# Performance work log

Measured on AMD Instinct MI355X. Metric: run time of the kernel, lower is better.

The kernel has to match this reference:

```python
import jax, jax.numpy as jnp
import numpy as np

C_ATOM = 128; C_PAIR = 16; H = 4; DH = 32; BQ = 32; BK = 128
N_ATOMS = 11776; NB = N_ATOMS // BQ; N_TOK = 512
C_TOK = 384; C_TP = 128; C_TP_IN = 32; N_LAYERS = 3

def _ln(x):
    mu = jnp.mean(x, axis=-1, keepdims=True)
    xc = x - mu
    var = jnp.mean(xc * xc, axis=-1, keepdims=True)
    return xc * jax.lax.rsqrt(var + 1e-5)

def setup_inputs():
    key = jax.random.key(0)
    ks = jax.random.split(key, 32)
    rn = lambda k, s, sc=0.02: jax.random.normal(k, s, jnp.float32) * sc
    q_idx = jnp.arange(N_ATOMS, dtype=jnp.int32).reshape(NB, BQ)
    centers = jnp.arange(NB, dtype=jnp.int32) * BQ + BQ // 2
    win = centers[:, None] + jnp.arange(-BK // 2, BK // 2, dtype=jnp.int32)[None, :]
    k_mask = (win >= 0) & (win < N_ATOMS)
    k_idx = jnp.clip(win, 0, N_ATOMS - 1)
    return {
        'atom_feats': jax.random.normal(ks[0], (1, N_ATOMS, C_ATOM), jnp.float32),
        'token_pair_feats': jax.random.normal(ks[1], (1, N_TOK, N_TOK, C_TP_IN), jnp.float32),
        'W_cond': rn(ks[2], (C_ATOM, C_ATOM)),
        'W_ph': rn(ks[3], (C_PAIR, C_ATOM)),
        'W_pw': rn(ks[4], (C_PAIR, C_ATOM)),
        'W_mlp1': rn(ks[5], (C_PAIR, C_PAIR)),
        'W_mlp2': rn(ks[6], (C_PAIR, C_PAIR)),
        'pb_ln_w': jnp.ones((C_PAIR,), jnp.float32),
        'pb_ln_b': jnp.zeros((C_PAIR,), jnp.float32),
        'pb_w': rn(ks[7], (H, C_PAIR)),
        'sln_w': rn(ks[8], (N_LAYERS, 2 * C_ATOM, C_ATOM)),
        'qkv_w': rn(ks[9], (N_LAYERS, 3 * C_ATOM, C_ATOM)),
        'q_bias': rn(ks[10], (N_LAYERS, C_ATOM)),
        'out_w': rn(ks[11], (N_LAYERS, C_ATOM, C_ATOM)),
        'out_b': jnp.zeros((N_LAYERS, C_ATOM), jnp.float32),
        'ada_w': rn(ks[12], (N_LAYERS, 2 * C_ATOM, C_ATOM)),
        'ta_w': rn(ks[13], (N_LAYERS, 4 * C_ATOM, C_ATOM)),
        'tb_w': rn(ks[14], (N_LAYERS, C_ATOM, 2 * C_ATOM)),
        'gate_w': rn(ks[15], (N_LAYERS, C_ATOM, C_ATOM)),
        'gate_b': jnp.full((N_LAYERS, C_ATOM), -2.0, jnp.float32),
        'W_tok': rn(ks[16], (C_TOK, C_ATOM)),
        'W_trunk': rn(ks[17], (C_TOK, C_TOK)),
        'W_struct': rn(ks[18], (C_TOK, C_TOK)),
        'W_pairin': rn(ks[19], (C_TP, C_TP_IN)),
        'W_outer': rn(ks[20], (2 * C_TP, C_TOK)),
        'q_idx': q_idx, 'k_idx': k_idx, 'k_mask': k_mask,
        'atom_to_token': jnp.sort(jax.random.randint(ks[21], (N_ATOMS,), 0, N_TOK, dtype=jnp.int32)),
    }

def _forward(atom_feats, token_pair_feats, W_cond, W_ph, W_pw, W_mlp1, W_mlp2,
             pb_ln_w, pb_ln_b, pb_w, sln_w, qkv_w, q_bias, out_w, out_b,
             ada_w, ta_w, tb_w, gate_w, gate_b, W_tok, W_trunk, W_struct,
             W_pairin, W_outer, q_idx, k_idx, k_mask, atom_to_token):
    c = atom_feats @ W_cond.T                       # [1,N,128] atom conditioning
    s_ln = _ln(c)                                   # shared normed conditioning
    # ---- blocked pair representation + pair-to-bias ----
    cq = jax.nn.relu(s_ln[:, q_idx])                # [1,NB,BQ,128]
    ck = jax.nn.relu(s_ln[:, k_idx])                # [1,NB,BK,128]
    p = (cq @ W_ph.T)[:, :, :, None, :] + (ck @ W_pw.T)[:, :, None, :, :]  # [1,NB,BQ,BK,16]
    p = p + jax.nn.relu(jax.nn.relu(p) @ W_mlp1.T) @ W_mlp2.T
    pb = (_ln(p) * pb_ln_w + pb_ln_b) @ pb_w.T      # [1,NB,BQ,BK,H]
    pb = jnp.transpose(pb, (0, 1, 4, 2, 3))         # [1,NB,H,BQ,BK]
    neg = jnp.where(k_mask[None, :, None, None, :], 0.0, -1e9)
    a = c
    scale = 1.0 / np.sqrt(DH).astype(np.float32)
    for l in range(N_LAYERS):
        # blocked local attention with AdaLN-conditioned input
        gb = s_ln @ sln_w[l].T
        x = jax.nn.sigmoid(gb[..., :C_ATOM]) * _ln(a) + gb[..., C_ATOM:]
        qkv = x @ qkv_w[l].T
        q, k, v = jnp.split(qkv, 3, axis=-1)
        q = (q + q_bias[l]).reshape(1, N_ATOMS, H, DH)
        k = k.reshape(1, N_ATOMS, H, DH)
        v = v.reshape(1, N_ATOMS, H, DH)
        qb = q[:, q_idx]; kb = k[:, k_idx]; vb = v[:, k_idx]
        sc = jnp.einsum('bnqhd,bnkhd->bnhqk', qb, kb) * scale + pb + neg
        att = jax.nn.softmax(sc, axis=-1)
        o = jnp.einsum('bnhqk,bnkhd->bnqhd', att, vb).reshape(1, N_ATOMS, C_ATOM)
        a = a + o @ out_w[l].T + out_b[l]
        # AdaLN-modulated SwiGLU transition with adaLN-zero gate (bias init -2)
        gb2 = s_ln @ ada_w[l].T
        xt = jax.nn.sigmoid(gb2[..., :C_ATOM]) * _ln(a) + gb2[..., C_ATOM:]
        ab = xt @ ta_w[l].T
        g = jax.nn.silu(ab[..., :2 * C_ATOM]) * ab[..., 2 * C_ATOM:]
        h = g @ tb_w[l].T
        gate = jax.nn.sigmoid(s_ln @ gate_w[l].T + gate_b[l])
        a = a + gate * h
    # ---- atom -> token aggregation and output projections ----
    atom_out = jax.nn.relu(a @ W_tok.T)             # [1,N,384]
    sums = jax.ops.segment_sum(atom_out[0], atom_to_token, num_segments=N_TOK)
    cnt = jax.ops.segment_sum(jnp.ones((N_ATOMS,), atom_out.dtype), atom_to_token, num_segments=N_TOK)
    tok = (sums / jnp.maximum(cnt, 1.0)[:, None])[None]  # [1,T,384]
    s_trunk = tok @ W_trunk.T
    s_struct = tok @ W_struct.T
    u = tok @ W_outer.T                              # [1,T,256]
    pair = token_pair_feats @ W_pairin.T + u[..., :C_TP][:, :, None, :] + u[..., C_TP:][:, None, :, :]
    return s_trunk, s_struct, pair

def reference(atom_feats, token_pair_feats, W_cond, W_ph, W_pw, W_mlp1, W_mlp2,
              pb_ln_w, pb_ln_b, pb_w, sln_w, qkv_w, q_bias, out_w, out_b,
              ada_w, ta_w, tb_w, gate_w, gate_b, W_tok, W_trunk, W_struct,
              W_pairin, W_outer, q_idx, k_idx, k_mask, atom_to_token):
    return _forward(atom_feats, token_pair_feats, W_cond, W_ph, W_pw, W_mlp1, W_mlp2,
                    pb_ln_w, pb_ln_b, pb_w, sln_w, qkv_w, q_bias, out_w, out_b,
                    ada_w, ta_w, tb_w, gate_w, gate_b, W_tok, W_trunk, W_struct,
                    W_pairin, W_outer, q_idx, k_idx, k_mask, atom_to_token)
```

## Files before the change

kernel.cpp:

```cpp
#include <hip/hip_runtime.h>
#include <cstddef>

typedef unsigned short u16;
typedef __attribute__((ext_vector_type(8))) short bf8;
typedef __attribute__((ext_vector_type(4))) float f4;
typedef __attribute__((ext_vector_type(4))) unsigned short us4;

#define NATOMS 11776
#define NBLK   368

__device__ __forceinline__ u16 f2b(float x){
  union { float f; unsigned u; } v; v.f = x;
  unsigned r = v.u + 0x7fffu + ((v.u >> 16) & 1u);
  return (u16)(r >> 16);
}
__device__ __forceinline__ float b2f(u16 x){
  union { unsigned u; float f; } v; v.u = ((unsigned)x) << 16;
  return v.f;
}
__device__ __forceinline__ f4 f4zero(){ f4 z = {0.f,0.f,0.f,0.f}; return z; }
__device__ __forceinline__ f4 mfma16(bf8 a, bf8 b, f4 c){
  return __builtin_amdgcn_mfma_f32_16x16x32_bf16(a, b, c, 0, 0, 0);
}
__device__ __forceinline__ int iclamp(int v, int lo, int hi){ return v < lo ? lo : (v > hi ? hi : v); }
__device__ __forceinline__ void lds_fence(){
  asm volatile("s_waitcnt lgkmcnt(0)" ::: "memory");
  __builtin_amdgcn_sched_barrier(0);
}
__device__ __forceinline__ bf8 cvt_f32x8(const float* __restrict__ p){
  float4 a = *(const float4*)p, b = *(const float4*)(p + 4);
  bf8 o;
  o[0] = (short)f2b(a.x); o[1] = (short)f2b(a.y); o[2] = (short)f2b(a.z); o[3] = (short)f2b(a.w);
  o[4] = (short)f2b(b.x); o[5] = (short)f2b(b.y); o[6] = (short)f2b(b.z); o[7] = (short)f2b(b.w);
  return o;
}

struct CvtArgs {
  const float* src[11];
  u16* dst[11];
  int n4[11];
};

__global__ __launch_bounds__(256) void k_convert(CvtArgs a){
  int stride = gridDim.x * 256;
  int tid = blockIdx.x * 256 + threadIdx.x;
  for (int s = 0; s < 11; ++s){
    const float4* src = (const float4*)a.src[s];
    us4* dst = (us4*)a.dst[s];
    int n = a.n4[s];
    for (int i = tid; i < n; i += stride){
      float4 v = src[i];
      us4 o;
      o.x = f2b(v.x); o.y = f2b(v.y); o.z = f2b(v.z); o.w = f2b(v.w);
      dst[i] = o;
    }
  }
}

template<int N, int K, int LDA = K>
__device__ __forceinline__ void gemm_strip(const u16* __restrict__ A, const u16* __restrict__ W, float* L){
  constexpr int CPW = N / 4;
  constexpr int T = CPW / 16;
  const int lane = threadIdx.x & 63;
  const int wave = threadIdx.x >> 6;
  const int rr = lane & 15, grp = lane >> 4;
  f4 acc[T];
#pragma unroll
  for (int t = 0; t < T; ++t) acc[t] = f4zero();
#pragma unroll
  for (int kc = 0; kc < K / 32; ++kc){
    bf8 af = *(const bf8*)(A + rr * LDA + kc * 32 + grp * 8);
#pragma unroll
    for (int t = 0; t < T; ++t){
      const u16* wp = W + (size_t)(wave * CPW + t * 16 + rr) * K + kc * 32 + grp * 8;
      acc[t] = mfma16(af, *(const bf8*)wp, acc[t]);
    }
  }
#pragma unroll
  for (int t = 0; t < T; ++t)
#pragma unroll
    for (int r = 0; r < 4; ++r)
      L[(grp * 4 + r) * N + wave * CPW + t * 16 + rr] = acc[t][r];
}

template<int LDA_A>
__device__ __forceinline__ void gemm_adaln(const u16* __restrict__ A, const u16* __restrict__ W,
                                           const float* __restrict__ LNf, u16* __restrict__ X){
  const int lane = threadIdx.x & 63;
  const int wave = threadIdx.x >> 6;
  const int rr = lane & 15, grp = lane >> 4;
  f4 acc[4];
#pragma unroll
  for (int t = 0; t < 4; ++t) acc[t] = f4zero();
#pragma unroll
  for (int kc = 0; kc < 4; ++kc){
    bf8 af = *(const bf8*)(A + rr * LDA_A + kc * 32 + grp * 8);
#pragma unroll
    for (int t = 0; t < 4; ++t){
      int col0 = (t < 2) ? wave * 32 + t * 16 : 128 + wave * 32 + (t - 2) * 16;
      acc[t] = mfma16(af, *(const bf8*)(W + (size_t)(col0 + rr) * 128 + kc * 32 + grp * 8), acc[t]);
    }
  }
#pragma unroll
  for (int t = 0; t < 2; ++t)
#pragma unroll
    for (int r = 0; r < 4; ++r){
      int row = grp * 4 + r, c = wave * 32 + t * 16 + rr;
      float s = 1.f / (1.f + __expf(-acc[t][r]));
      X[row * 136 + c] = f2b(s * LNf[row * 128 + c] + acc[t + 2][r]);
    }
}

__global__ __launch_bounds__(256) void k_cond_pre(const float* __restrict__ af, const float* __restrict__ Wc,
                                                  const float* __restrict__ Wph, const float* __restrict__ Wpw,
                                                  float* __restrict__ a_f, u16* __restrict__ sln_bf,
                                                  float* __restrict__ ph, float* __restrict__ pw,
                                                  const u16* __restrict__ slnW, const u16* __restrict__ qkvW,
                                                  const float* __restrict__ qb, u16* __restrict__ qkv_out){
  __shared__ float LB[16 * 384];
  __shared__ __align__(16) u16 Xs[16 * 136];
  __shared__ __align__(16) u16 Xr[16 * 136];
  __shared__ __align__(16) u16 Xx[16 * 136];
  __shared__ float LNf[16 * 128];
  const int strip = blockIdx.x;
  const int lane = threadIdx.x & 63, wave = threadIdx.x >> 6;
  const int rr = lane & 15, grp = lane >> 4;
  {
    f4 acc[2];
    acc[0] = f4zero(); acc[1] = f4zero();
#pragma unroll
    for (int kc = 0; kc < 4; ++kc){
      bf8 afr = cvt_f32x8(af + (size_t)(strip * 16 + rr) * 128 + kc * 32 + grp * 8);
#pragma unroll
      for (int t = 0; t < 2; ++t){
        bf8 bfr = cvt_f32x8(Wc + (size_t)(wave * 32 + t * 16 + rr) * 128 + kc * 32 + grp * 8);
        acc[t] = mfma16(afr, bfr, acc[t]);
      }
    }
#pragma unroll
    for (int t = 0; t < 2; ++t)
#pragma unroll
      for (int r = 0; r < 4; ++r)
        LB[(grp * 4 + r) * 128 + wave * 32 + t * 16 + rr] = acc[t][r];
  }
  __syncthreads();
  {
    int r = threadIdx.x >> 4, s = threadIdx.x & 15;
    float sum = 0.f, sq = 0.f;
#pragma unroll
    for (int j = 0; j < 8; ++j){ float v = LB[r * 128 + s * 8 + j]; sum += v; sq += v * v; }
#pragma unroll
    for (int m = 1; m < 16; m <<= 1){ sum += __shfl_xor(sum, m); sq += __shfl_xor(sq, m); }
    float mu = sum * (1.f / 128.f);
    float var = sq * (1.f / 128.f) - mu * mu;
    float rs = rsqrtf(var + 1e-5f);
#pragma unroll
    for (int j = 0; j < 8; ++j){
      int c = s * 8 + j;
      float v = LB[r * 128 + c];
      size_t idx = (size_t)(strip * 16 + r) * 128 + c;
      a_f[idx] = v;
      float ln = (v - mu) * rs;
      LNf[r * 128 + c] = ln;
      u16 lb = f2b(ln);
      sln_bf[idx] = lb;
      Xs[r * 136 + c] = lb;
      Xr[r * 136 + c] = f2b(fmaxf(ln, 0.f));
    }
  }
  __syncthreads();
  gemm_adaln<136>(Xs, slnW, LNf, Xx);
  __syncthreads();
  gemm_strip<384, 128, 136>(Xx, qkvW, LB);
  __syncthreads();
  const float scale = 0.17677669529663687f;
  for (int i = threadIdx.x; i < 16 * 384; i += 256){
    int r = i / 384, c = i - r * 384;
    float v = LB[i];
    if (c < 128) v = (v + qb[c]) * scale;
    qkv_out[(size_t)(strip * 16 + r) * 384 + c] = f2b(v);
  }
  if (wave < 2){
    const float* Wsel = wave ? Wpw : Wph;
    f4 acc = f4zero();
#pragma unroll
    for (int kc = 0; kc < 4; ++kc){
      bf8 afr = *(const bf8*)(&Xr[rr * 136 + kc * 32 + grp * 8]);
      bf8 bfr = cvt_f32x8(Wsel + (size_t)rr * 128 + kc * 32 + grp * 8);
      acc = mfma16(afr, bfr, acc);
    }
    float* out = wave ? pw : ph;
#pragma unroll
    for (int r = 0; r < 4; ++r)
      out[(size_t)(strip * 16 + grp * 4 + r) * 16 + rr] = acc[r];
  }
}

template<int LAST>
__global__ __launch_bounds__(256) void k_postpre(const u16* __restrict__ sln, const float* __restrict__ lnA,
                                                 float* __restrict__ a,
                                                 const u16* __restrict__ gateW, const float* __restrict__ gbias,
                                                 const u16* __restrict__ adaW, const u16* __restrict__ taW,
                                                 const u16* __restrict__ tbW,
                                                 const u16* __restrict__ slnW2, const u16* __restrict__ qkvW2,
                                                 const float* __restrict__ qb2, u16* __restrict__ qkv_out,
                                                 const u16* __restrict__ tokW, float* __restrict__ atom_out){
  __shared__ float LB[16 * 384];
  __shared__ __align__(16) u16 X[16 * 136];
  __shared__ __align__(16) u16 G[16 * 264];
  __shared__ float LNf[16 * 128];
  const int strip = blockIdx.x;
  const int lane = threadIdx.x & 63, wave = threadIdx.x >> 6;
  const int rr = lane & 15, grp = lane >> 4;
  const u16* Ag = sln + (size_t)strip * 2048;
  {
    f4 acc[6];
#pragma unroll
    for (int t = 0; t < 6; ++t) acc[t] = f4zero();
#pragma unroll
    for (int kc = 0; kc < 4; ++kc){
      bf8 af = *(const bf8*)(Ag + rr * 128 + kc * 32 + grp * 8);
#pragma unroll
      for (int t = 0; t < 6; ++t){
        int row0 = wave * 96 + t * 16;
        const u16* W = (row0 < 128) ? gateW + (size_t)(row0 + rr) * 128
                                    : adaW + (size_t)(row0 - 128 + rr) * 128;
        acc[t] = mfma16(af, *(const bf8*)(W + kc * 32 + grp * 8), acc[t]);
      }
    }
#pragma unroll
    for (int t = 0; t < 6; ++t)
#pragma unroll
      for (int r = 0; r < 4; ++r)
        LB[(grp * 4 + r) * 384 + wave * 96 + t * 16 + rr] = acc[t][r];
  }
  __syncthreads();
  float gv[8];
#pragma unroll
  for (int ii = 0; ii < 8; ++ii){
    int i = threadIdx.x + 256 * ii;
    int r = i >> 7, c = i & 127;
    gv[ii] = 1.f / (1.f + __expf(-(LB[r * 384 + c] + gbias[c])));
  }
  for (int i = threadIdx.x; i < 2048; i += 256){
    int r = i >> 7, c = i & 127;
    float g1 = LB[r * 384 + 128 + c], g2 = LB[r * 384 + 256 + c];
    float s = 1.f / (1.f + __expf(-g1));
    X[r * 136 + c] = f2b(s * lnA[(size_t)(strip * 16 + r) * 128 + c] + g2);
  }
  __syncthreads();
  {
    f4 acc[8];
#pragma unroll
    for (int t = 0; t < 8; ++t) acc[t] = f4zero();
#pragma unroll
    for (int kc = 0; kc < 4; ++kc){
      bf8 af = *(const bf8*)(&X[rr * 136 + kc * 32 + grp * 8]);
#pragma unroll
      for (int t = 0; t < 8; ++t){
        int col0 = (t < 4) ? wave * 64 + t * 16 : 256 + wave * 64 + (t - 4) * 16;
        acc[t] = mfma16(af, *(const bf8*)(taW + (size_t)(col0 + rr) * 128 + kc * 32 + grp * 8), acc[t]);
      }
    }
#pragma unroll
    for (int t = 0; t < 4; ++t)
#pragma unroll
      for (int r = 0; r < 4; ++r){
        float ab1 = acc[t][r], ab2 = acc[t + 4][r];
        G[(grp * 4 + r) * 264 + wave * 64 + t * 16 + rr] = f2b(ab1 / (1.f + __expf(-ab1)) * ab2);
      }
  }
  __syncthreads();
  gemm_strip<128, 256, 264>(G, tbW, LB);
  __syncthreads();
#pragma unroll
  for (int ii = 0; ii < 8; ++ii){
    int i = threadIdx.x + 256 * ii;
    size_t idx = (size_t)strip * 2048 + i;
    float v = a[idx] + gv[ii] * LB[i];
    a[idx] = v;
    LB[i] = v;
    if (LAST){ int r = i >> 7, c = i & 127; X[r * 136 + c] = f2b(v); }
  }
  __syncthreads();
  if (!LAST){
    {
      int r = threadIdx.x >> 4, s = threadIdx.x & 15;
      float sum = 0.f, sq = 0.f;
#pragma unroll
      for (int j = 0; j < 8; ++j){ float v = LB[r * 128 + s * 8 + j]; sum += v; sq += v * v; }
#pragma unroll
      for (int m = 1; m < 16; m <<= 1){ sum += __shfl_xor(sum, m); sq += __shfl_xor(sq, m); }
      float mu = sum * (1.f / 128.f);
      float var = sq * (1.f / 128.f) - mu * mu;
      float rs = rsqrtf(var + 1e-5f);
#pragma unroll
      for (int j = 0; j < 8; ++j){
        int c = s * 8 + j;
        LNf[r * 128 + c] = (LB[r * 128 + c] - mu) * rs;
      }
    }
    __syncthreads();
    gemm_adaln<128>(Ag, slnW2, LNf, X);
    __syncthreads();
    gemm_strip<384, 128, 136>(X, qkvW2, LB);
    __syncthreads();
    const float scale = 0.17677669529663687f;
    for (int i = threadIdx.x; i < 16 * 384; i += 256){
      int r = i / 384, c = i - r * 384;
      float v = LB[i];
      if (c < 128) v = (v + qb2[c]) * scale;
      qkv_out[(size_t)(strip * 16 + r) * 384 + c] = f2b(v);
    }
  } else {
    gemm_strip<384, 128, 136>(X, tokW, LB);
    __syncthreads();
    const size_t base = (size_t)strip * 16 * 384;
    for (int i = threadIdx.x; i < 16 * 384; i += 256) atom_out[base + i] = fmaxf(LB[i], 0.f);
  }
}

__global__ __launch_bounds__(256) void k_pb(const float* __restrict__ ph, const float* __restrict__ pw,
                                            const float* __restrict__ W1, const float* __restrict__ W2,
                                            const float* __restrict__ lnw, const float* __restrict__ lnb,
                                            const float* __restrict__ pbw, float* __restrict__ bias){
  __shared__ __align__(16) u16 mt[4][16 * 24];
  __shared__ __align__(16) u16 vt[4][16 * 24];
  const int t = threadIdx.x;
  const int lane = t & 63, wave = t >> 6;
  const int rr = lane & 15, grp = lane >> 4;
  const int b = blockIdx.x >> 3, qg = blockIdx.x & 7;
  const int q = qg * 4 + wave;
  const int qa = b * 32 + q;

  bf8 wf1 = {0,0,0,0,0,0,0,0}, wf2 = {0,0,0,0,0,0,0,0};
  bf8 bproj = {0,0,0,0,0,0,0,0}, bones = {0,0,0,0,0,0,0,0};
  if (grp < 2){
#pragma unroll
    for (int j = 0; j < 8; ++j){
      wf1[j] = (short)f2b(W1[rr * 16 + grp * 8 + j]);
      wf2[j] = (short)f2b(W2[rr * 16 + grp * 8 + j]);
      bones[j] = (short)0x3F80;
    }
    if (rr < 4){
#pragma unroll
      for (int j = 0; j < 8; ++j)
        bproj[j] = (short)f2b(pbw[rr * 16 + grp * 8 + j] * lnw[grp * 8 + j]);
    }
  }
  float w2s_r = 0.f, bb_r = 0.f;
  if (rr < 4){
#pragma unroll
    for (int cc = 0; cc < 16; ++cc){
      float pv = pbw[rr * 16 + cc];
      w2s_r += pv * lnw[cc];
      bb_r  += pv * lnb[cc];
    }
  }
  const float* phq = ph + (size_t)qa * 16;
  float pha[8];
  if (grp < 2){
#pragma unroll
    for (int j = 0; j < 8; ++j) pha[j] = phq[grp * 8 + j];
  }
  const float ph_r = phq[rr];
  u16* mw = &mt[wave][0];
  u16* vw = &vt[wave][0];

  for (int kt = 0; kt < 8; ++kt){
    const int k0 = kt * 16;
    bf8 af = {0,0,0,0,0,0,0,0};
    if (grp < 2){
      int winA = b * 32 + k0 + rr - 48;
      int kaA = iclamp(winA, 0, NATOMS - 1);
      const float* pwr = pw + (size_t)kaA * 16 + grp * 8;
#pragma unroll
      for (int j = 0; j < 8; ++j) af[j] = (short)f2b(fmaxf(pha[j] + pwr[j], 0.f));
    }
    f4 c1 = mfma16(af, wf1, f4zero());
#pragma unroll
    for (int r = 0; r < 4; ++r)
      mw[(grp * 4 + r) * 24 + rr] = f2b(fmaxf(c1[r], 0.f));
    lds_fence();
    bf8 mf = {0,0,0,0,0,0,0,0};
    if (grp < 2) mf = *(const bf8*)(mw + rr * 24 + grp * 8);
    f4 c2 = mfma16(mf, wf2, f4zero());
#pragma unroll
    for (int r = 0; r < 4; ++r){
      int win = b * 32 + k0 + grp * 4 + r - 48;
      int ka = iclamp(win, 0, NATOMS - 1);
      float v = c2[r] + ph_r + pw[(size_t)ka * 16 + rr];
      vw[(grp * 4 + r) * 24 + rr] = f2b(v);
    }
    lds_fence();
    bf8 vf = {0,0,0,0,0,0,0,0}, vf2 = {0,0,0,0,0,0,0,0};
    if (grp < 2){
      vf = *(const bf8*)(vw + rr * 24 + grp * 8);
#pragma unroll
      for (int j = 0; j < 8; ++j){
        float x = b2f((u16)vf[j]);
        union { float f; unsigned u; } s; s.f = x * x;
        vf2[j] = (short)(u16)(s.u >> 16);
      }
    }
    f4 T1 = mfma16(vf, bproj, f4zero());
    f4 T2 = mfma16(vf, bones, f4zero());
    f4 T3 = mfma16(vf2, bones, f4zero());
    if (rr < 4){
      float4 o;
      float ov[4];
#pragma unroll
      for (int r = 0; r < 4; ++r){
        int win = b * 32 + k0 + grp * 4 + r - 48;
        bool valid = (win >= 0) && (win < NATOMS);
        float S = T2[r], Q = T3[r], d = T1[r];
        float mu = S * (1.f / 16.f);
        float var = Q * (1.f / 16.f) - mu * mu;
        float rq = rsqrtf(var + 1e-5f);
        ov[r] = rq * (d - mu * w2s_r) + bb_r + (valid ? 0.f : -1e9f);
      }
      o.x = ov[0]; o.y = ov[1]; o.z = ov[2]; o.w = ov[3];
      *(float4*)(bias + ((size_t)((b * 4 + rr) * 32) + q) * 128 + k0 + grp * 4) = o;
    }
  }
}

__global__ __launch_bounds__(256) void k_attn(const u16* __restrict__ qkv, const float* __restrict__ bias,
                                              const u16* __restrict__ outw, const float* __restrict__ outb,
                                              float* __restrict__ a, float* __restrict__ lnA){
  __shared__ u16 VT[128][136];
  __shared__ u16 P[4][32 * 136];
  __shared__ u16 O[32][136];
  __shared__ float part2[32][8];
  const int t = threadIdx.x;
  const int lane = t & 63, wave = t >> 6;
  const int b = blockIdx.x;
  const int rr = lane & 15, grp = lane >> 4;

  for (int i = 0; i < 8; ++i){
    int s = t + 256 * i;
    int ka = s & 127, d0 = (s >> 7) * 8;
    int win = b * 32 + ka - 48;
    int src = iclamp(win, 0, NATOMS - 1);
    bf8 v = *(const bf8*)(qkv + (size_t)src * 384 + 256 + d0);
#pragma unroll
    for (int j = 0; j < 8; ++j) VT[d0 + j][ka] = (u16)v[j];
  }
  __syncthreads();

  const int h = wave;
  bf8 kfr[8];
#pragma unroll
  for (int kt = 0; kt < 8; ++kt){
    int ka = kt * 16 + rr;
    int win = b * 32 + ka - 48;
    int src = iclamp(win, 0, NATOMS - 1);
    kfr[kt] = *(const bf8*)(qkv + (size_t)src * 384 + 128 + h * 32 + grp * 8);
  }
  f4 S[2][8];
#pragma unroll
  for (int qt = 0; qt < 2; ++qt){
    bf8 qf = *(const bf8*)(qkv + (size_t)(b * 32 + qt * 16 + rr) * 384 + h * 32 + grp * 8);
#pragma unroll
    for (int kt = 0; kt < 8; ++kt){
      S[qt][kt] = f4zero();
      S[qt][kt] = mfma16(qf, kfr[kt], S[qt][kt]);
    }
  }
  const float* brow = bias + (size_t)((b * 4 + h) * 32) * 128;
#pragma unroll
  for (int qt = 0; qt < 2; ++qt){
#pragma unroll
    for (int r = 0; r < 4; ++r){
      int q = qt * 16 + grp * 4 + r;
      float vals[8];
      float mx = -1e30f;
#pragma unroll
      for (int kt = 0; kt < 8; ++kt){
        float v = S[qt][kt][r] + brow[q * 128 + kt * 16 + rr];
        vals[kt] = v;
        mx = fmaxf(mx, v);
      }
#pragma unroll
      for (int m = 1; m < 16; m <<= 1) mx = fmaxf(mx, __shfl_xor(mx, m));
      float sum = 0.f;
#pragma unroll
      for (int kt = 0; kt < 8; ++kt){ vals[kt] = __expf(vals[kt] - mx); sum += vals[kt]; }
#pragma unroll
      for (int m = 1; m < 16; m <<= 1) sum += __shfl_xor(sum, m);
      float inv = 1.f / sum;
#pragma unroll
      for (int kt = 0; kt < 8; ++kt)
        P[h][q * 136 + kt * 16 + rr] = f2b(vals[kt] * inv);
    }
  }
  __syncthreads();
  f4 oacc[2][2];
#pragma unroll
  for (int qt = 0; qt < 2; ++qt)
#pragma unroll
    for (int dt = 0; dt < 2; ++dt) oacc[qt][dt] = f4zero();
#pragma unroll
  for (int kc = 0; kc < 4; ++kc){
#pragma unroll
    for (int qt = 0; qt < 2; ++qt){
      bf8 pa = *(const bf8*)(&P[h][(qt * 16 + rr) * 136 + kc * 32 + grp * 8]);
#pragma unroll
      for (int dt = 0; dt < 2; ++dt){
        bf8 vb = *(const bf8*)(&VT[h * 32 + dt * 16 + rr][kc * 32 + grp * 8]);
        oacc[qt][dt] = mfma16(pa, vb, oacc[qt][dt]);
      }
    }
  }
#pragma unroll
  for (int qt = 0; qt < 2; ++qt)
#pragma unroll
    for (int dt = 0; dt < 2; ++dt)
#pragma unroll
      for (int r = 0; r < 4; ++r)
        O[qt * 16 + grp * 4 + r][h * 32 + dt * 16 + rr] = f2b(oacc[qt][dt][r]);
  __syncthreads();
  f4 pacc[2][2];
#pragma unroll
  for (int qt = 0; qt < 2; ++qt)
#pragma unroll
    for (int ct = 0; ct < 2; ++ct) pacc[qt][ct] = f4zero();
#pragma unroll
  for (int kc = 0; kc < 4; ++kc){
    bf8 a0 = *(const bf8*)(&O[rr][kc * 32 + grp * 8]);
    bf8 a1 = *(const bf8*)(&O[16 + rr][kc * 32 + grp * 8]);
#pragma unroll
    for (int ct = 0; ct < 2; ++ct){
      bf8 wf = *(const bf8*)(outw + (size_t)(wave * 32 + ct * 16 + rr) * 128 + kc * 32 + grp * 8);
      pacc[0][ct] = mfma16(a0, wf, pacc[0][ct]);
      pacc[1][ct] = mfma16(a1, wf, pacc[1][ct]);
    }
  }
  float vv[2][2][4];
#pragma unroll
  for (int qt = 0; qt < 2; ++qt)
#pragma unroll
    for (int ct = 0; ct < 2; ++ct)
#pragma unroll
      for (int r = 0; r < 4; ++r){
        int q = qt * 16 + grp * 4 + r;
        int col = wave * 32 + ct * 16 + rr;
        size_t idx = (size_t)(b * 32 + q) * 128 + col;
        float v = a[idx] + pacc[qt][ct][r] + outb[col];
        a[idx] = v;
        vv[qt][ct][r] = v;
      }
#pragma unroll
  for (int qt = 0; qt < 2; ++qt)
#pragma unroll
    for (int r = 0; r < 4; ++r){
      float ps = vv[qt][0][r] + vv[qt][1][r];
      float pq = vv[qt][0][r] * vv[qt][0][r] + vv[qt][1][r] * vv[qt][1][r];
#pragma unroll
      for (int m = 1; m < 16; m <<= 1){ ps += __shfl_xor(ps, m); pq += __shfl_xor(pq, m); }
      if (rr == 0){
        int q = qt * 16 + grp * 4 + r;
        part2[q][wave * 2] = ps;
        part2[q][wave * 2 + 1] = pq;
      }
    }
  __syncthreads();
#pragma unroll
  for (int qt = 0; qt < 2; ++qt)
#pragma unroll
    for (int r = 0; r < 4; ++r){
      int q = qt * 16 + grp * 4 + r;
      f4 p0 = *(const f4*)&part2[q][0];
      f4 p1 = *(const f4*)&part2[q][4];
      float S = p0[0] + p0[2] + p1[0] + p1[2];
      float Q = p0[1] + p0[3] + p1[1] + p1[3];
      float mu = S * (1.f / 128.f);
      float var = Q * (1.f / 128.f) - mu * mu;
      float rs = rsqrtf(var + 1e-5f);
#pragma unroll
      for (int ct = 0; ct < 2; ++ct){
        int col = wave * 32 + ct * 16 + rr;
        lnA[(size_t)(b * 32 + q) * 128 + col] = (vv[qt][ct][r] - mu) * rs;
      }
    }
}

__device__ __forceinline__ int lbound(const int* __restrict__ arr, int n, int v){
  int lo = 0, hi = n;
  while (lo < hi){ int mid = (lo + hi) >> 1; if (arr[mid] < v) lo = mid + 1; else hi = mid; }
  return lo;
}

__global__ __launch_bounds__(256) void k_segmean(const float* __restrict__ atom_out,
                                                 const int* __restrict__ a2t, u16* __restrict__ tokbf){
  const int tok = blockIdx.x;
  __shared__ int lo_s, hi_s;
  if (threadIdx.x == 0){
    lo_s = lbound(a2t, NATOMS, tok);
    hi_s = lbound(a2t, NATOMS, tok + 1);
  }
  __syncthreads();
  int lo = lo_s, hi = hi_s;
  float inv = 1.f / fmaxf((float)(hi - lo), 1.f);
  for (int c = threadIdx.x; c < 384; c += 256){
    float s = 0.f;
    for (int aa = lo; aa < hi; ++aa) s += atom_out[(size_t)aa * 384 + c];
    tokbf[(size_t)tok * 384 + c] = f2b(s * inv);
  }
}

__global__ __launch_bounds__(256) void k_tok(const u16* __restrict__ tok, const u16* __restrict__ catW,
                                             float* __restrict__ s_trunk, float* __restrict__ s_struct,
                                             float* __restrict__ u_f){
  __shared__ float LB[16 * 256];
  const int strip = blockIdx.x >> 2, quad = blockIdx.x & 3;
  gemm_strip<256, 384>(tok + (size_t)strip * 16 * 384, catW + (size_t)quad * 256 * 384, LB);
  __syncthreads();
  for (int i = threadIdx.x; i < 16 * 256; i += 256){
    int r = i >> 8, c = i & 255;
    int row = strip * 16 + r;
    int cg = quad * 256 + c;
    float v = LB[i];
    if (cg < 384) s_trunk[(size_t)row * 384 + cg] = v;
    else if (cg < 768) s_struct[(size_t)row * 384 + (cg - 384)] = v;
    else u_f[(size_t)row * 256 + (cg - 768)] = v;
  }
}

__global__ __launch_bounds__(256) void k_pair(const float* __restrict__ tpf, const float* __restrict__ Wp,
                                              const float* __restrict__ u, float* __restrict__ out){
  const int lane = threadIdx.x & 63, wave = threadIdx.x >> 6;
  const int rr = lane & 15, grp = lane >> 4;
  const int pairbase = blockIdx.x * 64 + wave * 16;
  const int i = (blockIdx.x * 64) >> 9;
  bf8 af;
  {
    const float* tr = tpf + (size_t)(pairbase + rr) * 32 + grp * 8;
#pragma unroll
    for (int j = 0; j < 8; ++j) af[j] = (short)f2b(tr[j]);
  }
  f4 acc[8];
#pragma unroll
  for (int t = 0; t < 8; ++t){
    bf8 bf;
    const float* wr = Wp + (size_t)(t * 16 + rr) * 32 + grp * 8;
#pragma unroll
    for (int j = 0; j < 8; ++j) bf[j] = (short)f2b(wr[j]);
    acc[t] = mfma16(af, bf, f4zero());
  }
  const float* ui = u + (size_t)i * 256;
#pragma unroll
  for (int t = 0; t < 8; ++t){
    int c = t * 16 + rr;
    float uic = ui[c];
#pragma unroll
    for (int r = 0; r < 4; ++r){
      int p = pairbase + grp * 4 + r;
      int j = p & 511;
      out[(size_t)p * 128 + c] = acc[t][r] + uic + u[(size_t)j * 256 + 128 + c];
    }
  }
}

extern "C" void kernel_launch(void* const* d_in, const int* in_sizes, int n_in,
                              void* d_out, int out_size, void* d_ws, size_t ws_size,
                              hipStream_t stream){
  (void)in_sizes; (void)n_in; (void)out_size; (void)ws_size;
  const float* atom_feats = (const float*)d_in[0];
  const float* tpf        = (const float*)d_in[1];
  const float* W_cond     = (const float*)d_in[2];
  const float* W_ph       = (const float*)d_in[3];
  const float* W_pw       = (const float*)d_in[4];
  const float* W_mlp1     = (const float*)d_in[5];
  const float* W_mlp2     = (const float*)d_in[6];
  const float* pb_ln_w    = (const float*)d_in[7];
  const float* pb_ln_b    = (const float*)d_in[8];
  const float* pb_w       = (const float*)d_in[9];
  const float* sln_w      = (const float*)d_in[10];
  const float* qkv_w      = (const float*)d_in[11];
  const float* q_bias     = (const float*)d_in[12];
  const float* out_w      = (const float*)d_in[13];
  const float* out_b      = (const float*)d_in[14];
  const float* ada_w      = (const float*)d_in[15];
  const float* ta_w       = (const float*)d_in[16];
  const float* tb_w       = (const float*)d_in[17];
  const float* gate_w     = (const float*)d_in[18];
  const float* gate_b     = (const float*)d_in[19];
  const float* W_tok      = (const float*)d_in[20];
  const float* W_trunk    = (const float*)d_in[21];
  const float* W_struct   = (const float*)d_in[22];
  const float* W_pairin   = (const float*)d_in[23];
  const float* W_outer    = (const float*)d_in[24];
  const int*   a2t        = (const int*)d_in[28];

  char* wsb = (char*)d_ws;
  size_t off = 0;
  auto alc = [&](size_t bytes) -> void* {
    void* r = wsb + off;
    off = (off + bytes + 255) & ~(size_t)255;
    return r;
  };

  u16* sln_bfw   = (u16*)alc(98304 * 2);
  u16* qkv_bfw   = (u16*)alc(147456 * 2);
  u16* out_bfw   = (u16*)alc(49152 * 2);
  u16* ada_bfw   = (u16*)alc(98304 * 2);
  u16* ta_bfw    = (u16*)alc(196608 * 2);
  u16* tb_bfw    = (u16*)alc(98304 * 2);
  u16* gate_bfw  = (u16*)alc(49152 * 2);
  u16* tok_bfw   = (u16*)alc(49152 * 2);
  u16* trunk_bfw = (u16*)alc(147456 * 2);
  u16* struct_bfw= (u16*)alc(147456 * 2);
  u16* outer_bfw = (u16*)alc(98304 * 2);
  float* a_f     = (float*)alc((size_t)NATOMS * 128 * 4);
  float* lnA     = (float*)alc((size_t)NATOMS * 128 * 4);
  u16* sln_bf    = (u16*)alc((size_t)NATOMS * 128 * 2);
  u16* qkv_bf    = (u16*)alc((size_t)NATOMS * 384 * 2);
  float* ph      = (float*)alc((size_t)NATOMS * 16 * 4);
  float* pw      = (float*)alc((size_t)NATOMS * 16 * 4);
  float* bias    = (float*)alc((size_t)NBLK * 4 * 32 * 128 * 4);
  float* atom_out= bias;
  u16* tok_bf    = (u16*)alc(512 * 384 * 2);
  float* u_f     = (float*)alc(512 * 256 * 4);

  float* s_trunk  = (float*)d_out;
  float* s_struct = s_trunk + 512 * 384;
  float* pair_out = s_struct + 512 * 384;

  CvtArgs ca;
  const float* srcs[11] = {sln_w, qkv_w, out_w, ada_w, ta_w, tb_w, gate_w,
                           W_tok, W_trunk, W_struct, W_outer};
  u16* dsts[11] = {sln_bfw, qkv_bfw, out_bfw, ada_bfw, ta_bfw, tb_bfw, gate_bfw,
                   tok_bfw, trunk_bfw, struct_bfw, outer_bfw};
  int n4s[11] = {24576, 36864, 12288, 24576, 49152, 24576, 12288,
                 12288, 36864, 36864, 24576};
  for (int s = 0; s < 11; ++s){ ca.src[s] = srcs[s]; ca.dst[s] = dsts[s]; ca.n4[s] = n4s[s]; }
  k_convert<<<256, 256, 0, stream>>>(ca);

  k_cond_pre<<<736, 256, 0, stream>>>(atom_feats, W_cond, W_ph, W_pw, a_f, sln_bf, ph, pw,
                                      sln_bfw, qkv_bfw, q_bias, qkv_bf);
  k_pb<<<NBLK * 8, 256, 0, stream>>>(ph, pw, W_mlp1, W_mlp2, pb_ln_w, pb_ln_b, pb_w, bias);

  for (int l = 0; l < 3; ++l){
    const u16* outW  = out_bfw  + (size_t)l * 128 * 128;
    const u16* adaW  = ada_bfw  + (size_t)l * 256 * 128;
    const u16* taW   = ta_bfw   + (size_t)l * 512 * 128;
    const u16* tbW   = tb_bfw   + (size_t)l * 128 * 256;
    const u16* gateW = gate_bfw + (size_t)l * 128 * 128;
    k_attn<<<NBLK, 256, 0, stream>>>(qkv_bf, bias, outW, out_b + l * 128, a_f, lnA);
    if (l < 2){
      const u16* slnW2 = sln_bfw + (size_t)(l + 1) * 256 * 128;
      const u16* qkvW2 = qkv_bfw + (size_t)(l + 1) * 384 * 128;
      k_postpre<0><<<736, 256, 0, stream>>>(sln_bf, lnA, a_f, gateW, gate_b + l * 128,
                                            adaW, taW, tbW, slnW2, qkvW2,
                                            q_bias + (l + 1) * 128, qkv_bf,
                                            nullptr, nullptr);
    } else {
      k_postpre<1><<<736, 256, 0, stream>>>(sln_bf, lnA, a_f, gateW, gate_b + l * 128,
                                            adaW, taW, tbW, nullptr, nullptr,
                                            nullptr, nullptr,
                                            tok_bfw, atom_out);
    }
  }

  k_segmean<<<512, 256, 0, stream>>>(atom_out, a2t, tok_bf);
  k_tok<<<128, 256, 0, stream>>>(tok_bf, trunk_bfw, s_trunk, s_struct, u_f);
  k_pair<<<4096, 256, 0, stream>>>(tpf, W_pairin, u_f, pair_out);
}
```

Baseline: 356.0 us.

## Run k_postpre with 512 threads, splitting GEMM columns across eight waves

Doubles the k_postpre block from 4 to 8 waves. Each wave now computes half as many output column tiles in every GEMM stage, and the elementwise and layernorm loops are re-strided for 512 threads. The adaLN GEMM is inlined with the per-wave split. The goal is more latency hiding and shorter per-wave serial MFMA chains for this small 16-row strip kernel. The cost is more waves competing for LDS and barriers, and lower occupancy per CU at 512 threads.

```diff
diff --git a/kernel.cpp b/kernel.cpp
--- a/kernel.cpp
+++ b/kernel.cpp
@@ -57,9 +57,9 @@
   }
 }
 
-template<int N, int K, int LDA = K>
+template<int N, int K, int LDA = K, int NW = 4>
 __device__ __forceinline__ void gemm_strip(const u16* __restrict__ A, const u16* __restrict__ W, float* L){
-  constexpr int CPW = N / 4;
+  constexpr int CPW = N / NW;
   constexpr int T = CPW / 16;
   const int lane = threadIdx.x & 63;
   const int wave = threadIdx.x >> 6;
@@ -197,7 +197,7 @@
 }
 
 template<int LAST>
-__global__ __launch_bounds__(256) void k_postpre(const u16* __restrict__ sln, const float* __restrict__ lnA,
+__global__ __launch_bounds__(512) void k_postpre(const u16* __restrict__ sln, const float* __restrict__ lnA,
                                                  float* __restrict__ a,
                                                  const u16* __restrict__ gateW, const float* __restrict__ gbias,
                                                  const u16* __restrict__ adaW, const u16* __restrict__ taW,
@@ -210,39 +210,40 @@
   __shared__ __align__(16) u16 G[16 * 264];
   __shared__ float LNf[16 * 128];
   const int strip = blockIdx.x;
-  const int lane = threadIdx.x & 63, wave = threadIdx.x >> 6;
+  const int t = threadIdx.x;
+  const int lane = t & 63, wave = t >> 6;
   const int rr = lane & 15, grp = lane >> 4;
   const u16* Ag = sln + (size_t)strip * 2048;
   {
-    f4 acc[6];
-#pragma unroll
-    for (int t = 0; t < 6; ++t) acc[t] = f4zero();
+    f4 acc[3];
+#pragma unroll
+    for (int tt = 0; tt < 3; ++tt) acc[tt] = f4zero();
 #pragma unroll
     for (int kc = 0; kc < 4; ++kc){
       bf8 af = *(const bf8*)(Ag + rr * 128 + kc * 32 + grp * 8);
 #pragma unroll
-      for (int t = 0; t < 6; ++t){
-        int row0 = wave * 96 + t * 16;
+      for (int tt = 0; tt < 3; ++tt){
+        int row0 = wave * 48 + tt * 16;
         const u16* W = (row0 < 128) ? gateW + (size_t)(row0 + rr) * 128
                                     : adaW + (size_t)(row0 - 128 + rr) * 128;
-        acc[t] = mfma16(af, *(const bf8*)(W + kc * 32 + grp * 8), acc[t]);
-      }
-    }
-#pragma unroll
-    for (int t = 0; t < 6; ++t)
+        acc[tt] = mfma16(af, *(const bf8*)(W + kc * 32 + grp * 8), acc[tt]);
+      }
+    }
+#pragma unroll
+    for (int tt = 0; tt < 3; ++tt)
 #pragma unroll
       for (int r = 0; r < 4; ++r)
-        LB[(grp * 4 + r) * 384 + wave * 96 + t * 16 + rr] = acc[t][r];
-  }
-  __syncthreads();
-  float gv[8];
-#pragma unroll
-  for (int ii = 0; ii < 8; ++ii){
-    int i = threadIdx.x + 256 * ii;
+        LB[(grp * 4 + r) * 384 + wave * 48 + tt * 16 + rr] = acc[tt][r];
+  }
+  __syncthreads();
+  float gv[4];
+#pragma unroll
+  for (int ii = 0; ii < 4; ++ii){
+    int i = t + 512 * ii;
     int r = i >> 7, c = i & 127;
     gv[ii] = 1.f / (1.f + __expf(-(LB[r * 384 + c] + gbias[c])));
   }
-  for (int i = threadIdx.x; i < 2048; i += 256){
+  for (int i = t; i < 2048; i += 512){
     int r = i >> 7, c = i & 127;
     float g1 = LB[r * 384 + 128 + c], g2 = LB[r * 384 + 256 + c];
     float s = 1.f / (1.f + __expf(-g1));
@@ -250,32 +251,32 @@
   }
   __syncthreads();
   {
-    f4 acc[8];
-#pragma unroll
-    for (int t = 0; t < 8; ++t) acc[t] = f4zero();
+    f4 acc[4];
+#pragma unroll
+    for (int tt = 0; tt < 4; ++tt) acc[tt] = f4zero();
 #pragma unroll
     for (int kc = 0; kc < 4; ++kc){
       bf8 af = *(const bf8*)(&X[rr * 136 + kc * 32 + grp * 8]);
 #pragma unroll
-      for (int t = 0; t < 8; ++t){
-        int col0 = (t < 4) ? wave * 64 + t * 16 : 256 + wave * 64 + (t - 4) * 16;
-        acc[t] = mfma16(af, *(const bf8*)(taW + (size_t)(col0 + rr) * 128 + kc * 32 + grp * 8), acc[t]);
-      }
-    }
-#pragma unroll
-    for (int t = 0; t < 4; ++t)
+      for (int tt = 0; tt < 4; ++tt){
+        int col0 = (tt < 2) ? wave * 32 + tt * 16 : 256 + wave * 32 + (tt - 2) * 16;
+        acc[tt] = mfma16(af, *(const bf8*)(taW + (size_t)(col0 + rr) * 128 + kc * 32 + grp * 8), acc[tt]);
+      }
+    }
+#pragma unroll
+    for (int tt = 0; tt < 2; ++tt)
 #pragma unroll
       for (int r = 0; r < 4; ++r){
-        float ab1 = acc[t][r], ab2 = acc[t + 4][r];
-        G[(grp * 4 + r) * 264 + wave * 64 + t * 16 + rr] = f2b(ab1 / (1.f + __expf(-ab1)) * ab2);
-      }
-  }
-  __syncthreads();
-  gemm_strip<128, 256, 264>(G, tbW, LB);
-  __syncthreads();
-#pragma unroll
-  for (int ii = 0; ii < 8; ++ii){
-    int i = threadIdx.x + 256 * ii;
+        float ab1 = acc[tt][r], ab2 = acc[tt + 2][r];
+        G[(grp * 4 + r) * 264 + wave * 32 + tt * 16 + rr] = f2b(ab1 / (1.f + __expf(-ab1)) * ab2);
+      }
+  }
+  __syncthreads();
+  gemm_strip<128, 256, 264, 8>(G, tbW, LB);
+  __syncthreads();
+#pragma unroll
+  for (int ii = 0; ii < 4; ++ii){
+    int i = t + 512 * ii;
     size_t idx = (size_t)strip * 2048 + i;
     float v = a[idx] + gv[ii] * LB[i];
     a[idx] = v;
@@ -285,38 +286,52 @@
   __syncthreads();
   if (!LAST){
     {
-      int r = threadIdx.x >> 4, s = threadIdx.x & 15;
+      int r = t >> 5, s = t & 31;
       float sum = 0.f, sq = 0.f;
 #pragma unroll
-      for (int j = 0; j < 8; ++j){ float v = LB[r * 128 + s * 8 + j]; sum += v; sq += v * v; }
-#pragma unroll
-      for (int m = 1; m < 16; m <<= 1){ sum += __shfl_xor(sum, m); sq += __shfl_xor(sq, m); }
+      for (int j = 0; j < 4; ++j){ float v = LB[r * 128 + s * 4 + j]; sum += v; sq += v * v; }
+#pragma unroll
+      for (int m = 1; m < 32; m <<= 1){ sum += __shfl_xor(sum, m); sq += __shfl_xor(sq, m); }
       float mu = sum * (1.f / 128.f);
       float var = sq * (1.f / 128.f) - mu * mu;
       float rs = rsqrtf(var + 1e-5f);
 #pragma unroll
-      for (int j = 0; j < 8; ++j){
-        int c = s * 8 + j;
+      for (int j = 0; j < 4; ++j){
+        int c = s * 4 + j;
         LNf[r * 128 + c] = (LB[r * 128 + c] - mu) * rs;
       }
     }
     __syncthreads();
-    gemm_adaln<128>(Ag, slnW2, LNf, X);
+    {
+      f4 acc0 = f4zero(), acc1 = f4zero();
+#pragma unroll
+      for (int kc = 0; kc < 4; ++kc){
+        bf8 af = *(const bf8*)(Ag + rr * 128 + kc * 32 + grp * 8);
+        acc0 = mfma16(af, *(const bf8*)(slnW2 + (size_t)(wave * 16 + rr) * 128 + kc * 32 + grp * 8), acc0);
+        acc1 = mfma16(af, *(const bf8*)(slnW2 + (size_t)(128 + wave * 16 + rr) * 128 + kc * 32 + grp * 8), acc1);
+      }
+#pragma unroll
+      for (int r = 0; r < 4; ++r){
+        int row = grp * 4 + r, c = wave * 16 + rr;
+        float s = 1.f / (1.f + __expf(-acc0[r]));
+        X[row * 136 + c] = f2b(s * LNf[row * 128 + c] + acc1[r]);
+      }
+    }
     __syncthreads();
-    gemm_strip<384, 128, 136>(X, qkvW2, LB);
+    gemm_strip<384, 128, 136, 8>(X, qkvW2, LB);
     __syncthreads();
     const float scale = 0.17677669529663687f;
-    for (int i = threadIdx.x; i < 16 * 384; i += 256){
+    for (int i = t; i < 16 * 384; i += 512){
       int r = i / 384, c = i - r * 384;
       float v = LB[i];
       if (c < 128) v = (v + qb2[c]) * scale;
       qkv_out[(size_t)(strip * 16 + r) * 384 + c] = f2b(v);
     }
   } else {
-    gemm_strip<384, 128, 136>(X, tokW, LB);
+    gemm_strip<384, 128, 136, 8>(X, tokW, LB);
     __syncthreads();
     const size_t base = (size_t)strip * 16 * 384;
-    for (int i = threadIdx.x; i < 16 * 384; i += 256) atom_out[base + i] = fmaxf(LB[i], 0.f);
+    for (int i = t; i < 16 * 384; i += 512) atom_out[base + i] = fmaxf(LB[i], 0.f);
   }
 }
 
@@ -751,12 +766,12 @@
     if (l < 2){
       const u16* slnW2 = sln_bfw + (size_t)(l + 1) * 256 * 128;
       const u16* qkvW2 = qkv_bfw + (size_t)(l + 1) * 384 * 128;
-      k_postpre<0><<<736, 256, 0, stream>>>(sln_bf, lnA, a_f, gateW, gate_b + l * 128,
+      k_postpre<0><<<736, 512, 0, stream>>>(sln_bf, lnA, a_f, gateW, gate_b + l * 128,
                                             adaW, taW, tbW, slnW2, qkvW2,
                                             q_bias + (l + 1) * 128, qkv_bf,
                                             nullptr, nullptr);
     } else {
-      k_postpre<1><<<736, 256, 0, stream>>>(sln_bf, lnA, a_f, gateW, gate_b + l * 128,
+      k_postpre<1><<<736, 512, 0, stream>>>(sln_bf, lnA, a_f, gateW, gate_b + l * 128,
                                             adaW, taW, tbW, nullptr, nullptr,
                                             nullptr, nullptr,
                                             tok_bfw, atom_out);
```

Result: no change. 356.9 us (+0.3%).
